# Performance work log

Hardware: AMD Instinct MI355X
Metric: run time of the kernel (lower is better)

Reference implementation:

```python
import jax, jax.numpy as jnp
import numpy as np

BATCH, SEQ, IN_DIM, N_NODES = 32, 2048, 256, 256


def setup_inputs() -> dict:
    key = jax.random.key(0)
    k1, k2, k3 = jax.random.split(key, 3)
    x = jax.random.normal(k1, (BATCH * SEQ, IN_DIM), dtype=jnp.float32)
    h0 = jnp.zeros((BATCH, N_NODES), dtype=jnp.float32)
    # TF GRUCell kernels (glorot-ish scale), gate bias init = 1.0 as in TF
    W_g = jax.random.normal(k2, (IN_DIM + N_NODES, 2 * N_NODES), dtype=jnp.float32) * 0.05
    b_g = jnp.ones((2 * N_NODES,), dtype=jnp.float32)
    W_c = jax.random.normal(k3, (IN_DIM + N_NODES, N_NODES), dtype=jnp.float32) * 0.05
    b_c = jnp.zeros((N_NODES,), dtype=jnp.float32)
    return {"x": x, "h0": h0, "W_g": W_g, "b_g": b_g, "W_c": W_c, "b_c": b_c}


def reference(x, h0, W_g, b_g, W_c, b_c):
    B, N = h0.shape
    D = x.shape[-1]
    seq = x.reshape(B, -1, D)              # [B, T, D]
    xs = jnp.swapaxes(seq, 0, 1)           # [T, B, D] for scan over time

    def step(h, xt):
        gi = jnp.concatenate([xt, h], axis=-1)                 # [B, D+N]
        gates = jax.nn.sigmoid(gi @ W_g + b_g)                 # [B, 2N]
        r, u = jnp.split(gates, 2, axis=-1)
        ci = jnp.concatenate([xt, r * h], axis=-1)             # [B, D+N]
        c = jnp.tanh(ci @ W_c + b_c)                           # [B, N]
        h_new = u * h + (1.0 - u) * c
        return h_new, h_new

    _, ys = jax.lax.scan(step, h0, xs)      # ys: [T, B, N]
    out = jnp.swapaxes(ys, 0, 1).reshape(-1, N)  # [B*T, N] like tf.reshape(outputs, [-1, nNodes])
    return out
```

## Files before the change

kernel.cpp:

```cpp
#include <hip/hip_runtime.h>
#include <hip/hip_fp16.h>

#define SEQ   2048
#define IND   256
#define NN    256

typedef _Float16 h2_t __attribute__((ext_vector_type(2)));

__device__ __forceinline__ float dot2f(unsigned a, unsigned b, float c) {
#if __has_builtin(__builtin_amdgcn_fdot2)
  union { unsigned u; h2_t h; } ua, ub;
  ua.u = a; ub.u = b;
  return __builtin_amdgcn_fdot2(ua.h, ub.h, c, false);
#else
  union { unsigned u; __half2 h; } ua, ub;
  ua.u = a; ub.u = b;
  return fmaf(__low2float(ua.h), __low2float(ub.h),
              fmaf(__high2float(ua.h), __high2float(ub.h), c));
#endif
}

__device__ __forceinline__ float fast_sigmoid(float x) {
  float e = __expf(-x);
  return __builtin_amdgcn_rcpf(1.f + e);
}
__device__ __forceinline__ float fast_tanh(float x) {
  x = fminf(15.f, fmaxf(-15.f, x));
  float e = __expf(2.f * x);
  return (e - 1.f) * __builtin_amdgcn_rcpf(e + 1.f);
}

__global__ void pack_weights(const float* __restrict__ Wg,
                             const float* __restrict__ Wc,
                             unsigned* __restrict__ WGH,
                             unsigned* __restrict__ WCH) {
  int idx = blockIdx.x * 256 + threadIdx.x;
  if (idx < 512 * 128) {
    int col = idx >> 7, k2 = idx & 127;
    __half2 p = __floats2half2_rn(Wg[(256 + 2 * k2) * 512 + col],
                                  Wg[(257 + 2 * k2) * 512 + col]);
    union { __half2 h; unsigned u; } cv; cv.h = p;
    WGH[idx] = cv.u;
  } else {
    int i2 = idx - 512 * 128;
    int n = i2 >> 7, k2 = i2 & 127;
    __half2 p = __floats2half2_rn(Wc[(256 + 2 * k2) * 256 + n],
                                  Wc[(257 + 2 * k2) * 256 + n]);
    union { __half2 h; unsigned u; } cv; cv.h = p;
    WCH[i2] = cv.u;
  }
}

__global__ __launch_bounds__(256) void xproj_gemm(
    const float* __restrict__ x, const float* __restrict__ Wg,
    const float* __restrict__ Wc, __half* XG, __half* XC) {
  __shared__ float As[16][68];
  __shared__ float Bs[16][64];
  const int i0 = blockIdx.x * 64;
  const int j0 = blockIdx.y * 64;
  const int tid = threadIdx.x;
  const int tr = tid >> 4, tc = tid & 15;
  const int arow = tid >> 2, ac4 = (tid & 3) * 4;
  const int bk = tid >> 4, bj4 = (tid & 15) * 4;
  const bool isG = (j0 < 512);
  const float* B = isG ? Wg : Wc;
  const int ldb = isG ? 512 : 256;
  const int jb  = (isG ? j0 : (j0 - 512)) + bj4;
  float acc[4][4] = {};
  for (int k0 = 0; k0 < IND; k0 += 16) {
    float4 av = *(const float4*)&x[(size_t)(i0 + arow) * IND + k0 + ac4];
    As[ac4+0][arow] = av.x; As[ac4+1][arow] = av.y;
    As[ac4+2][arow] = av.z; As[ac4+3][arow] = av.w;
    *(float4*)&Bs[bk][bj4] = *(const float4*)&B[(size_t)(k0 + bk) * ldb + jb];
    __syncthreads();
#pragma unroll
    for (int k = 0; k < 16; ++k) {
      float4 a4 = *(const float4*)&As[k][tr * 4];
      float4 b4 = *(const float4*)&Bs[k][tc * 4];
      float a[4] = {a4.x, a4.y, a4.z, a4.w};
      float b[4] = {b4.x, b4.y, b4.z, b4.w};
#pragma unroll
      for (int r = 0; r < 4; ++r)
#pragma unroll
        for (int c = 0; c < 4; ++c) acc[r][c] = fmaf(a[r], b[c], acc[r][c]);
    }
    __syncthreads();
  }
  for (int r = 0; r < 4; ++r) {
    const size_t i = i0 + tr * 4 + r;
    const int j = j0 + tc * 4;
    __half2 p0 = __floats2half2_rn(acc[r][0], acc[r][1]);
    __half2 p1 = __floats2half2_rn(acc[r][2], acc[r][3]);
    union { __half2 h2[2]; uint2 u; } pk; pk.h2[0] = p0; pk.h2[1] = p1;
    if (isG) *(uint2*)&XG[i * 512 + j]         = pk.u;
    else     *(uint2*)&XC[i * 256 + (j - 512)] = pk.u;
  }
}

__global__ __launch_bounds__(512) void gru_scan(
    const unsigned* __restrict__ WGH, const unsigned* __restrict__ WCH,
    const float* __restrict__ bg, const float* __restrict__ bc,
    const float* __restrict__ h0,
    const __half* __restrict__ XG, const __half* __restrict__ XC,
    float* __restrict__ out) {
  __shared__ unsigned h2[128];
  __shared__ unsigned rh2[128];
  const int b  = blockIdx.x;
  const int j  = threadIdx.x;
  const int n  = j >> 1;
  const int kh = j & 1;
  const int gcol = kh ? (n + 256) : n;

  unsigned wg[128];
  {
    const uint4* p = (const uint4*)(WGH + (size_t)gcol * 128);
#pragma unroll
    for (int i = 0; i < 32; ++i) ((uint4*)wg)[i] = p[i];
  }
  unsigned wc[64];
  {
    const uint4* p = (const uint4*)(WCH + (size_t)n * 128 + (size_t)kh * 64);
#pragma unroll
    for (int i = 0; i < 16; ++i) ((uint4*)wc)[i] = p[i];
  }

  const float bgj = bg[gcol];
  const float bcn = bc[n];
  float hn = h0[b * NN + n];
  if (kh == 0) ((__half*)h2)[n] = __float2half_rn(hn);
  __syncthreads();

  const size_t rowbase = (size_t)b * SEQ;
  for (int t = 0; t < SEQ; ++t) {
    const size_t row = rowbase + t;
    const __half xgh = XG[row * 512 + gcol];
    __half xch = __float2half_rn(0.f);
    if (kh == 0) xch = XC[row * 256 + n];

    float a0 = 0.f, a1 = 0.f, a2 = 0.f, a3 = 0.f;
    const uint4* h4 = (const uint4*)h2;
#pragma unroll
    for (int c = 0; c < 32; ++c) {
      uint4 hv = h4[c];
      a0 = dot2f(wg[4 * c + 0], hv.x, a0);
      a1 = dot2f(wg[4 * c + 1], hv.y, a1);
      a2 = dot2f(wg[4 * c + 2], hv.z, a2);
      a3 = dot2f(wg[4 * c + 3], hv.w, a3);
    }
    float g = fast_sigmoid(bgj + __half2float(xgh) + ((a0 + a1) + (a2 + a3)));
    float ex = __shfl_xor(g, 1);
    float r = kh ? ex : g;
    float u = kh ? g : ex;
    if (kh == 0) ((__half*)rh2)[n] = __float2half_rn(r * hn);
    __syncthreads();

    float c0 = 0.f, c1 = 0.f, c2 = 0.f, c3 = 0.f;
    const uint4* r4 = (const uint4*)rh2 + kh * 16;
#pragma unroll
    for (int c = 0; c < 16; ++c) {
      uint4 rv = r4[c];
      c0 = dot2f(wc[4 * c + 0], rv.x, c0);
      c1 = dot2f(wc[4 * c + 1], rv.y, c1);
      c2 = dot2f(wc[4 * c + 2], rv.z, c2);
      c3 = dot2f(wc[4 * c + 3], rv.w, c3);
    }
    float cacc = (c0 + c1) + (c2 + c3);
    if (kh == 0) cacc += bcn + __half2float(xch);
    cacc += __shfl_xor(cacc, 1);
    const float cc = fast_tanh(cacc);
    hn = u * hn + (1.f - u) * cc;
    if (kh == 0) {
      out[row * 256 + n] = hn;
      ((__half*)h2)[n] = __float2half_rn(hn);
    }
    __syncthreads();
  }
}

extern "C" void kernel_launch(void* const* d_in, const int* in_sizes, int n_in,
                              void* d_out, int out_size, void* d_ws, size_t ws_size,
                              hipStream_t stream) {
  const float* x  = (const float*)d_in[0];
  const float* h0 = (const float*)d_in[1];
  const float* Wg = (const float*)d_in[2];
  const float* bg = (const float*)d_in[3];
  const float* Wc = (const float*)d_in[4];
  const float* bc = (const float*)d_in[5];

  char* ws = (char*)d_ws;
  __half*   XC  = (__half*)ws;
  unsigned* WGH = (unsigned*)(ws + 33554432);
  unsigned* WCH = (unsigned*)(ws + 33816576);
  __half*   XG  = (__half*)d_out;
  float*    out = (float*)d_out;

  hipLaunchKernelGGL(pack_weights, dim3(384), dim3(256), 0, stream, Wg, Wc, WGH, WCH);
  hipLaunchKernelGGL(xproj_gemm, dim3(1024, 12), dim3(256), 0, stream, x, Wg, Wc, XG, XC);
  hipLaunchKernelGGL(gru_scan, dim3(32), dim3(512), 0, stream,
                     WGH, WCH, bg, bc, h0, XG, XC, out);
}
```

Before: 3.678 ms.

## Split GRU scan dot products over K across waves with LDS reduction

Each wave in the recurrent scan now owns a 16-element half2 K-slice and computes partial dot products for 8 gate columns and 4 candidate columns. Partial sums are combined through padded shared-memory arrays. Weights are repacked to match this layout, and the update gate is passed to the candidate stage through shared memory. The aim is to cut per-thread broadcast reads of the full hidden state from LDS on each step. In exchange it adds an extra barrier and an LDS reduction per step, and it keeps 192 weight registers per thread.

```diff
diff --git a/kernel.cpp b/kernel.cpp
--- a/kernel.cpp
+++ b/kernel.cpp
@@ -32,23 +32,31 @@
 
 __global__ void pack_weights(const float* __restrict__ Wg,
                              const float* __restrict__ Wc,
-                             unsigned* __restrict__ WGH,
-                             unsigned* __restrict__ WCH) {
+                             unsigned* __restrict__ PK) {
   int idx = blockIdx.x * 256 + threadIdx.x;
-  if (idx < 512 * 128) {
-    int col = idx >> 7, k2 = idx & 127;
-    __half2 p = __floats2half2_rn(Wg[(256 + 2 * k2) * 512 + col],
-                                  Wg[(257 + 2 * k2) * 512 + col]);
-    union { __half2 h; unsigned u; } cv; cv.h = p;
-    WGH[idx] = cv.u;
+  int s4  = idx >> 11;
+  int rem = idx & 2047;
+  int t   = rem >> 2;
+  int slot = s4 * 4 + (rem & 3);
+  int w = t >> 6, l = t & 63;
+  float lo, hi;
+  if (slot < 128) {
+    int i = slot >> 4, k = slot & 15;
+    int col = l + 64 * i;
+    int k2 = 16 * w + k;
+    lo = Wg[(256 + 2 * k2) * 512 + col];
+    hi = Wg[(257 + 2 * k2) * 512 + col];
   } else {
-    int i2 = idx - 512 * 128;
-    int n = i2 >> 7, k2 = i2 & 127;
-    __half2 p = __floats2half2_rn(Wc[(256 + 2 * k2) * 256 + n],
-                                  Wc[(257 + 2 * k2) * 256 + n]);
-    union { __half2 h; unsigned u; } cv; cv.h = p;
-    WCH[i2] = cv.u;
-  }
+    int s = slot - 128;
+    int i = s >> 4, k = s & 15;
+    int n = l + 64 * i;
+    int k2 = 16 * w + k;
+    lo = Wc[(256 + 2 * k2) * 256 + n];
+    hi = Wc[(257 + 2 * k2) * 256 + n];
+  }
+  union { __half2 h; unsigned u; } cv;
+  cv.h = __floats2half2_rn(lo, hi);
+  PK[idx] = cv.u;
 }
 
 __global__ __launch_bounds__(256) void xproj_gemm(
@@ -97,81 +105,93 @@
   }
 }
 
-__global__ __launch_bounds__(512) void gru_scan(
-    const unsigned* __restrict__ WGH, const unsigned* __restrict__ WCH,
+__global__ __launch_bounds__(512, 2) void gru_scan(
+    const unsigned* __restrict__ PK,
     const float* __restrict__ bg, const float* __restrict__ bc,
     const float* __restrict__ h0,
     const __half* __restrict__ XG, const __half* __restrict__ XC,
     float* __restrict__ out) {
-  __shared__ unsigned h2[128];
-  __shared__ unsigned rh2[128];
-  const int b  = blockIdx.x;
-  const int j  = threadIdx.x;
-  const int n  = j >> 1;
-  const int kh = j & 1;
-  const int gcol = kh ? (n + 256) : n;
-
-  unsigned wg[128];
+  __shared__ unsigned h2s[128];
+  __shared__ unsigned rh2s[128];
+  __shared__ float pG[512 * 9];
+  __shared__ float pC[256 * 9];
+  __shared__ float uarr[256];
+  const int b    = blockIdx.x;
+  const int tid  = threadIdx.x;
+  const int wave = tid >> 6, lane = tid & 63;
+
+  unsigned wreg[192];
   {
-    const uint4* p = (const uint4*)(WGH + (size_t)gcol * 128);
-#pragma unroll
-    for (int i = 0; i < 32; ++i) ((uint4*)wg)[i] = p[i];
-  }
-  unsigned wc[64];
-  {
-    const uint4* p = (const uint4*)(WCH + (size_t)n * 128 + (size_t)kh * 64);
-#pragma unroll
-    for (int i = 0; i < 16; ++i) ((uint4*)wc)[i] = p[i];
-  }
-
-  const float bgj = bg[gcol];
-  const float bcn = bc[n];
-  float hn = h0[b * NN + n];
-  if (kh == 0) ((__half*)h2)[n] = __float2half_rn(hn);
+    const uint4* p = (const uint4*)PK + tid;
+#pragma unroll
+    for (int s4 = 0; s4 < 48; ++s4) ((uint4*)wreg)[s4] = p[s4 * 512];
+  }
+#pragma unroll
+  for (int i = 0; i < 192; ++i) asm volatile("" : "+v"(wreg[i]));
+
+  const float bgj = bg[tid];
+  const float bcn = (tid < 256) ? bc[tid] : 0.f;
+  float hn = 0.f;
+  if (tid < 256) {
+    hn = h0[b * NN + tid];
+    ((__half*)h2s)[tid] = __float2half_rn(hn);
+  }
   __syncthreads();
 
   const size_t rowbase = (size_t)b * SEQ;
   for (int t = 0; t < SEQ; ++t) {
     const size_t row = rowbase + t;
-    const __half xgh = XG[row * 512 + gcol];
-    __half xch = __float2half_rn(0.f);
-    if (kh == 0) xch = XC[row * 256 + n];
-
-    float a0 = 0.f, a1 = 0.f, a2 = 0.f, a3 = 0.f;
-    const uint4* h4 = (const uint4*)h2;
-#pragma unroll
-    for (int c = 0; c < 32; ++c) {
-      uint4 hv = h4[c];
-      a0 = dot2f(wg[4 * c + 0], hv.x, a0);
-      a1 = dot2f(wg[4 * c + 1], hv.y, a1);
-      a2 = dot2f(wg[4 * c + 2], hv.z, a2);
-      a3 = dot2f(wg[4 * c + 3], hv.w, a3);
-    }
-    float g = fast_sigmoid(bgj + __half2float(xgh) + ((a0 + a1) + (a2 + a3)));
-    float ex = __shfl_xor(g, 1);
-    float r = kh ? ex : g;
-    float u = kh ? g : ex;
-    if (kh == 0) ((__half*)rh2)[n] = __float2half_rn(r * hn);
-    __syncthreads();
-
-    float c0 = 0.f, c1 = 0.f, c2 = 0.f, c3 = 0.f;
-    const uint4* r4 = (const uint4*)rh2 + kh * 16;
-#pragma unroll
-    for (int c = 0; c < 16; ++c) {
-      uint4 rv = r4[c];
-      c0 = dot2f(wc[4 * c + 0], rv.x, c0);
-      c1 = dot2f(wc[4 * c + 1], rv.y, c1);
-      c2 = dot2f(wc[4 * c + 2], rv.z, c2);
-      c3 = dot2f(wc[4 * c + 3], rv.w, c3);
-    }
-    float cacc = (c0 + c1) + (c2 + c3);
-    if (kh == 0) cacc += bcn + __half2float(xch);
-    cacc += __shfl_xor(cacc, 1);
-    const float cc = fast_tanh(cacc);
-    hn = u * hn + (1.f - u) * cc;
-    if (kh == 0) {
-      out[row * 256 + n] = hn;
-      ((__half*)h2)[n] = __float2half_rn(hn);
+    const float xg = __half2float(XG[row * 512 + tid]);
+    float xc = 0.f;
+    if (tid < 256) xc = __half2float(XC[row * 256 + tid]);
+
+    unsigned hk[16];
+    {
+      const uint4* hb = (const uint4*)h2s + wave * 4;
+      ((uint4*)hk)[0] = hb[0]; ((uint4*)hk)[1] = hb[1];
+      ((uint4*)hk)[2] = hb[2]; ((uint4*)hk)[3] = hb[3];
+    }
+#pragma unroll
+    for (int i = 0; i < 8; ++i) {
+      float pa = 0.f;
+#pragma unroll
+      for (int k = 0; k < 16; ++k) pa = dot2f(wreg[i * 16 + k], hk[k], pa);
+      pG[(lane + 64 * i) * 9 + wave] = pa;
+    }
+    __syncthreads();
+
+    float s = bgj + xg;
+#pragma unroll
+    for (int w = 0; w < 8; ++w) s += pG[tid * 9 + w];
+    const float g = fast_sigmoid(s);
+    if (tid < 256) ((__half*)rh2s)[tid] = __float2half_rn(g * hn);
+    else           uarr[tid - 256] = g;
+    __syncthreads();
+
+    unsigned rk[16];
+    {
+      const uint4* rb = (const uint4*)rh2s + wave * 4;
+      ((uint4*)rk)[0] = rb[0]; ((uint4*)rk)[1] = rb[1];
+      ((uint4*)rk)[2] = rb[2]; ((uint4*)rk)[3] = rb[3];
+    }
+#pragma unroll
+    for (int i = 0; i < 4; ++i) {
+      float pc = 0.f;
+#pragma unroll
+      for (int k = 0; k < 16; ++k) pc = dot2f(wreg[128 + i * 16 + k], rk[k], pc);
+      pC[(lane + 64 * i) * 9 + wave] = pc;
+    }
+    __syncthreads();
+
+    if (tid < 256) {
+      float sc = bcn + xc;
+#pragma unroll
+      for (int w = 0; w < 8; ++w) sc += pC[tid * 9 + w];
+      const float c = fast_tanh(sc);
+      const float u = uarr[tid];
+      hn = u * hn + (1.f - u) * c;
+      out[row * 256 + tid] = hn;
+      ((__half*)h2s)[tid] = __float2half_rn(hn);
     }
     __syncthreads();
   }
@@ -188,14 +208,13 @@
   const float* bc = (const float*)d_in[5];
 
   char* ws = (char*)d_ws;
-  __half*   XC  = (__half*)ws;
-  unsigned* WGH = (unsigned*)(ws + 33554432);
-  unsigned* WCH = (unsigned*)(ws + 33816576);
-  __half*   XG  = (__half*)d_out;
+  __half*   XC = (__half*)ws;
+  unsigned* PK = (unsigned*)(ws + 33554432);
+  __half*   XG = (__half*)d_out;
   float*    out = (float*)d_out;
 
-  hipLaunchKernelGGL(pack_weights, dim3(384), dim3(256), 0, stream, Wg, Wc, WGH, WCH);
+  hipLaunchKernelGGL(pack_weights, dim3(384), dim3(256), 0, stream, Wg, Wc, PK);
   hipLaunchKernelGGL(xproj_gemm, dim3(1024, 12), dim3(256), 0, stream, x, Wg, Wc, XG, XC);
   hipLaunchKernelGGL(gru_scan, dim3(32), dim3(512), 0, stream,
-                     WGH, WCH, bg, bc, h0, XG, XC, out);
-}
+                     PK, bg, bc, h0, XG, XC, out);
+}
```

Result: faster. 3.475 ms (-5.5%).
